# Kernel tuning notes

Measured on AMD Instinct MI355X. Metric: run time of the kernel, lower is better.

The kernel has to match this reference:

```python
import jax, jax.numpy as jnp
import numpy as np

NEG_INF = -9e15
LEAKY_SLOPE = 0.01  # PyTorch F.leaky_relu default


def setup_inputs() -> dict:
    key = jax.random.key(0)
    k1, k2, k3, k4 = jax.random.split(key, 4)
    B, N, Fin, Fout = 4, 4096, 64, 64
    X = jax.random.normal(k1, (B, N, Fin), dtype=jnp.float32)
    A = jax.random.randint(k2, (N, N), 0, 2, dtype=jnp.int32)
    weight = jax.random.normal(k3, (Fin, Fout), dtype=jnp.float32) * 0.15
    a = jax.random.normal(k4, (2 * Fout, 1), dtype=jnp.float32) * 0.15
    return {"X": X, "A": A, "weight": weight, "a": a}


def reference(X, A, weight, a):
    B, N, _ = X.shape
    Fout = weight.shape[1]
    # add self loops: A[i,i] = 1
    mask = (A > 0) | jnp.eye(N, dtype=bool)  # [N, N]
    Xw = jnp.matmul(X, weight)  # [B, N, Fout]
    # additive attention: e_ij = leaky_relu(a_l . x_i + a_r . x_j)
    # equivalent to the repeat/cat/matmul in the original, without O(N^2 F) memory
    a_l = a[:Fout, 0]   # [Fout]
    a_r = a[Fout:, 0]   # [Fout]
    left = jnp.einsum('bnf,f->bn', Xw, a_l)   # [B, N]
    right = jnp.einsum('bnf,f->bn', Xw, a_r)  # [B, N]
    e = left[:, :, None] + right[:, None, :]  # [B, N, N]
    e = jnp.where(e >= 0, e, LEAKY_SLOPE * e)
    att = jnp.where(mask[None, :, :], e, NEG_INF)
    att = jax.nn.softmax(att, axis=-1)  # dropout p=0 -> identity
    out = jnp.matmul(att, Xw)  # [B, N, Fout]
    return out
```

## Files before the change

kernel.cpp:

```cpp
#include <hip/hip_runtime.h>
#include <hip/hip_bf16.h>
#include <math.h>

#define BB 4
#define NN 4096
#define FF 64
#define KS (NN / 32)
#define NKW (KS / 4)
#define C0F 3.35462628e-4f
#define C1F 3.35462628e-6f

typedef _Float16 half8 __attribute__((ext_vector_type(8)));
typedef float f32x4 __attribute__((ext_vector_type(4)));

__global__ void k_pack(const int* __restrict__ A, unsigned int* __restrict__ bitsT) {
    int idx = blockIdx.x * 256 + threadIdx.x;
    int row = idx >> 12;
    int col = idx & (NN - 1);
    bool pred = (A[idx] > 0) || (row == col);
    unsigned long long m = __ballot(pred);
    int lane = threadIdx.x & 63;
    if (lane == 0)  bitsT[(size_t)(col >> 5) * NN + row] = (unsigned int)(m & 0xffffffffULL);
    if (lane == 32) bitsT[(size_t)(col >> 5) * NN + row] = (unsigned int)(m >> 32);
}

__global__ __launch_bounds__(256, 2)
void k_pre(const float* __restrict__ X, const float* __restrict__ W,
           const float* __restrict__ avec, _Float16* __restrict__ XwP,
           float2* __restrict__ LE, float2* __restrict__ RE) {
    __shared__ __align__(16) float Wl[64 * 64];
    __shared__ __align__(16) float Xl[32][64];
    __shared__ __align__(16) float T[32][65];
    __shared__ float al[64];
    __shared__ float ar[64];
    const int t = threadIdx.x;
    const int lane = t & 63;
    const int wv = t >> 6;
    const int r0 = blockIdx.x * 32;

    #pragma unroll
    for (int k = 0; k < 16; ++k) Wl[t + k * 256] = W[t + k * 256];
    if (t < 64) { al[t] = avec[t]; ar[t] = avec[64 + t]; }
    {
        const float4* xs = (const float4*)(X + (size_t)r0 * 64);
        float4* xd = (float4*)&Xl[0][0];
        xd[t] = xs[t];
        xd[t + 256] = xs[t + 256];
    }
    __syncthreads();

    float Wreg[64];
    #pragma unroll
    for (int k = 0; k < 64; ++k) Wreg[k] = Wl[k * 64 + lane];

    #pragma unroll
    for (int rr = 0; rr < 8; ++rr) {
        int lrow = wv * 8 + rr;
        int row  = r0 + lrow;
        float a0 = 0.f, a1 = 0.f, a2 = 0.f, a3 = 0.f;
        #pragma unroll
        for (int k = 0; k < 64; k += 4) {
            float4 x = *(const float4*)&Xl[lrow][k];
            a0 = fmaf(x.x, Wreg[k],     a0);
            a1 = fmaf(x.y, Wreg[k + 1], a1);
            a2 = fmaf(x.z, Wreg[k + 2], a2);
            a3 = fmaf(x.w, Wreg[k + 3], a3);
        }
        float acc = (a0 + a1) + (a2 + a3);
        T[lrow][lane] = acc;

        float lv = acc * al[lane];
        float rv = acc * ar[lane];
        #pragma unroll
        for (int off = 32; off; off >>= 1) {
            lv += __shfl_xor(lv, off, 64);
            rv += __shfl_xor(rv, off, 64);
        }
        if (lane == 0) {
            LE[row] = make_float2(lv, __expf(lv - 8.f));
            RE[row] = make_float2(rv, __expf(rv));
        }
    }
    __syncthreads();

    int b  = r0 >> 12;
    int ks = (r0 & (NN - 1)) >> 5;
    int ct = t >> 6;
    int q  = lane >> 4, n = lane & 15;
    half8 h;
    #pragma unroll
    for (int jj = 0; jj < 8; ++jj)
        h[jj] = (_Float16)T[q * 8 + jj][ct * 16 + n];
    *(half8*)&XwP[((((size_t)b * KS + ks) * 4 + ct) * 64 + lane) * 8] = h;
}

__global__ __launch_bounds__(256, 2)
void k_main(const _Float16* __restrict__ XwP, const float2* __restrict__ LE,
            const float2* __restrict__ RE, const unsigned int* __restrict__ bitsT,
            float* __restrict__ out) {
    __shared__ __align__(16) char smem[32768];
    float2* REs = (float2*)smem;
    float (*Lacc)[32][68] = (float (*)[32][68])smem;
    float* Lsum = (float*)(smem + 17408);

    const int t  = threadIdx.x;
    const int b  = blockIdx.y;
    const int i0 = blockIdx.x * 32;

    const int lane = t & 63;
    const int wv   = t >> 6;
    const int lm   = lane & 15;
    const int q    = lane >> 4;

    const int rowa = i0 + lm;
    const int rowb = i0 + 16 + lm;
    const float2 lea = LE[b * NN + rowa];
    const float2 leb = LE[b * NN + rowb];
    const _Float16* xp = XwP + (size_t)b * KS * 2048 + (size_t)lane * 8;

    {
        const float4* rsrc = (const float4*)(RE + (size_t)b * NN);
        float4* rdst = (float4*)REs;
        #pragma unroll
        for (int k = 0; k < 8; ++k) rdst[t + k * 256] = rsrc[t + k * 256];
    }
    __syncthreads();

    f32x4 acca[4], accb[4];
    f32x4 sacca = (f32x4)0.f, saccb = (f32x4)0.f;
    #pragma unroll
    for (int ct = 0; ct < 4; ++ct) { acca[ct] = (f32x4)0.f; accb[ct] = (f32x4)0.f; }
    half8 vones;
    #pragma unroll
    for (int k = 0; k < 8; ++k) vones[k] = (_Float16)1.0f;

    const int ks0 = wv * NKW;

    const _Float16* base = xp + (size_t)ks0 * 2048;
    half8 nb0 = *(const half8*)(base + 0 * 512);
    half8 nb1 = *(const half8*)(base + 1 * 512);
    half8 nb2 = *(const half8*)(base + 2 * 512);
    half8 nb3 = *(const half8*)(base + 3 * 512);
    unsigned int nwa = bitsT[(size_t)ks0 * NN + rowa];
    unsigned int nwb = bitsT[(size_t)ks0 * NN + rowb];

    #pragma unroll 2
    for (int kk = 0; kk < NKW; ++kk) {
        half8 bf0 = nb0, bf1 = nb1, bf2 = nb2, bf3 = nb3;
        unsigned int wa = nwa >> (q * 8);
        unsigned int wb = nwb >> (q * 8);

        {
            int nk = kk + 1 < NKW ? kk + 1 : kk;
            const _Float16* nbase = xp + (size_t)(ks0 + nk) * 2048;
            nb0 = *(const half8*)(nbase + 0 * 512);
            nb1 = *(const half8*)(nbase + 1 * 512);
            nb2 = *(const half8*)(nbase + 2 * 512);
            nb3 = *(const half8*)(nbase + 3 * 512);
            nwa = bitsT[(size_t)(ks0 + nk) * NN + rowa];
            nwb = bitsT[(size_t)(ks0 + nk) * NN + rowb];
        }

        const float4* rp = (const float4*)(REs + (ks0 + kk) * 32 + q * 8);
        float4 ra = rp[0], rb = rp[1], rc = rp[2], rd = rp[3];
        float r8[8]  = {ra.x, ra.z, rb.x, rb.z, rc.x, rc.z, rd.x, rd.z};
        float er8[8] = {ra.y, ra.w, rb.y, rb.w, rc.y, rc.w, rd.y, rd.w};

        half8 a0a, a0b;
        #pragma unroll
        for (int jj = 0; jj < 8; ++jj) {
            float e0 = lea.x + r8[jj];
            float p0 = fmaxf(lea.y * er8[jj], fmaf(e0, C1F, C0F));
            p0 = ((wa >> jj) & 1u) ? p0 : 0.f;
            a0a[jj] = (_Float16)p0;
        }
        acca[0] = __builtin_amdgcn_mfma_f32_16x16x32_f16(a0a, bf0, acca[0], 0, 0, 0);
        acca[1] = __builtin_amdgcn_mfma_f32_16x16x32_f16(a0a, bf1, acca[1], 0, 0, 0);
        acca[2] = __builtin_amdgcn_mfma_f32_16x16x32_f16(a0a, bf2, acca[2], 0, 0, 0);
        acca[3] = __builtin_amdgcn_mfma_f32_16x16x32_f16(a0a, bf3, acca[3], 0, 0, 0);
        sacca   = __builtin_amdgcn_mfma_f32_16x16x32_f16(a0a, vones, sacca, 0, 0, 0);

        #pragma unroll
        for (int jj = 0; jj < 8; ++jj) {
            float e0 = leb.x + r8[jj];
            float p0 = fmaxf(leb.y * er8[jj], fmaf(e0, C1F, C0F));
            p0 = ((wb >> jj) & 1u) ? p0 : 0.f;
            a0b[jj] = (_Float16)p0;
        }
        accb[0] = __builtin_amdgcn_mfma_f32_16x16x32_f16(a0b, bf0, accb[0], 0, 0, 0);
        accb[1] = __builtin_amdgcn_mfma_f32_16x16x32_f16(a0b, bf1, accb[1], 0, 0, 0);
        accb[2] = __builtin_amdgcn_mfma_f32_16x16x32_f16(a0b, bf2, accb[2], 0, 0, 0);
        accb[3] = __builtin_amdgcn_mfma_f32_16x16x32_f16(a0b, bf3, accb[3], 0, 0, 0);
        saccb   = __builtin_amdgcn_mfma_f32_16x16x32_f16(a0b, vones, saccb, 0, 0, 0);
    }

    __syncthreads();

    if (wv >= 2) {
        #pragma unroll
        for (int r = 0; r < 4; ++r) {
            int lrow = q * 4 + r;
            #pragma unroll
            for (int ct = 0; ct < 4; ++ct) {
                Lacc[wv - 2][lrow][ct * 16 + lm]      = acca[ct][r];
                Lacc[wv - 2][16 + lrow][ct * 16 + lm] = accb[ct][r];
            }
            if (lm == 0) {
                Lsum[(wv - 2) * 32 + lrow]      = sacca[r];
                Lsum[(wv - 2) * 32 + 16 + lrow] = saccb[r];
            }
        }
    }
    __syncthreads();
    if (wv < 2) {
        #pragma unroll
        for (int r = 0; r < 4; ++r) {
            int lrow = q * 4 + r;
            #pragma unroll
            for (int ct = 0; ct < 4; ++ct) {
                Lacc[wv][lrow][ct * 16 + lm]      += acca[ct][r];
                Lacc[wv][16 + lrow][ct * 16 + lm] += accb[ct][r];
            }
            if (lm == 0) {
                Lsum[wv * 32 + lrow]      += sacca[r];
                Lsum[wv * 32 + 16 + lrow] += saccb[r];
            }
        }
    }
    __syncthreads();
    #pragma unroll
    for (int it = 0; it < 2; ++it) {
        int idx  = t + it * 256;
        int lrow = idx >> 4;
        int c0   = (idx & 15) * 4;
        float s = Lsum[lrow] + Lsum[32 + lrow];
        float inv = 1.f / s;
        float4 o;
        o.x = (Lacc[0][lrow][c0 + 0] + Lacc[1][lrow][c0 + 0]) * inv;
        o.y = (Lacc[0][lrow][c0 + 1] + Lacc[1][lrow][c0 + 1]) * inv;
        o.z = (Lacc[0][lrow][c0 + 2] + Lacc[1][lrow][c0 + 2]) * inv;
        o.w = (Lacc[0][lrow][c0 + 3] + Lacc[1][lrow][c0 + 3]) * inv;
        *(float4*)&out[((size_t)(b * NN + i0 + lrow) << 6) + c0] = o;
    }
}

extern "C" void kernel_launch(void* const* d_in, const int* in_sizes, int n_in,
                              void* d_out, int out_size, void* d_ws, size_t ws_size,
                              hipStream_t stream) {
    const float* X    = (const float*)d_in[0];
    const int*   A    = (const int*)d_in[1];
    const float* W    = (const float*)d_in[2];
    const float* avec = (const float*)d_in[3];
    float* out = (float*)d_out;

    char* ws = (char*)d_ws;
    size_t off = 0;
    _Float16* XwP = (_Float16*)(ws + off); off += (size_t)BB * NN * FF * 2;
    float2* LE = (float2*)(ws + off);      off += (size_t)BB * NN * 8;
    float2* RE = (float2*)(ws + off);      off += (size_t)BB * NN * 8;
    unsigned int* bitsT = (unsigned int*)(ws + off);
    off += (size_t)KS * NN * 4;
    (void)off; (void)ws_size;

    k_pack<<<NN * NN / 256, 256, 0, stream>>>(A, bitsT);
    k_pre<<<BB * NN / 32, 256, 0, stream>>>(X, W, avec, XwP, LE, RE);
    k_main<<<dim3(NN / 32, BB), 256, 0, stream>>>(XwP, LE, RE, bitsT, out);
}
```

Baseline: 147.4 us.

## Merge mask packing into preprocessing kernel with vectorized uint4 loads

Folds the adjacency bit-packing kernel into the feature preprocessing kernel as extra blocks, removing one launch. The packing path now loads four ints per thread as uint4 and combines nibbles with a few xor shuffles instead of one ballot per element, so it needs a quarter of the threads. The cost is a heavier combined kernel whose shared-memory footprint also applies to the packing blocks, which may lower their occupancy.

```diff
diff --git a/kernel.cpp b/kernel.cpp
--- a/kernel.cpp
+++ b/kernel.cpp
@@ -9,31 +9,46 @@
 #define NKW (KS / 4)
 #define C0F 3.35462628e-4f
 #define C1F 3.35462628e-6f
+#define PREB 512
 
 typedef _Float16 half8 __attribute__((ext_vector_type(8)));
 typedef float f32x4 __attribute__((ext_vector_type(4)));
 
-__global__ void k_pack(const int* __restrict__ A, unsigned int* __restrict__ bitsT) {
-    int idx = blockIdx.x * 256 + threadIdx.x;
-    int row = idx >> 12;
-    int col = idx & (NN - 1);
-    bool pred = (A[idx] > 0) || (row == col);
-    unsigned long long m = __ballot(pred);
-    int lane = threadIdx.x & 63;
-    if (lane == 0)  bitsT[(size_t)(col >> 5) * NN + row] = (unsigned int)(m & 0xffffffffULL);
-    if (lane == 32) bitsT[(size_t)(col >> 5) * NN + row] = (unsigned int)(m >> 32);
-}
-
 __global__ __launch_bounds__(256, 2)
-void k_pre(const float* __restrict__ X, const float* __restrict__ W,
-           const float* __restrict__ avec, _Float16* __restrict__ XwP,
-           float2* __restrict__ LE, float2* __restrict__ RE) {
+void k_prep(const float* __restrict__ X, const float* __restrict__ W,
+            const float* __restrict__ avec, const int* __restrict__ A,
+            _Float16* __restrict__ XwP, float2* __restrict__ LE,
+            float2* __restrict__ RE, unsigned int* __restrict__ bitsT) {
     __shared__ __align__(16) float Wl[64 * 64];
     __shared__ __align__(16) float Xl[32][64];
     __shared__ __align__(16) float T[32][65];
     __shared__ float al[64];
     __shared__ float ar[64];
+
     const int t = threadIdx.x;
+
+    if (blockIdx.x >= PREB) {
+        int pidx = (blockIdx.x - PREB) * 256 + t;
+        int row  = pidx >> 10;
+        int c4   = pidx & 1023;
+        const uint4* A4 = (const uint4*)A;
+        uint4 av = A4[pidx];
+        unsigned int nib = 0;
+        nib |= ((int)av.x > 0) ? 1u : 0u;
+        nib |= ((int)av.y > 0) ? 2u : 0u;
+        nib |= ((int)av.z > 0) ? 4u : 0u;
+        nib |= ((int)av.w > 0) ? 8u : 0u;
+        if (c4 == (row >> 2)) nib |= 1u << (row & 3);
+        int lane = t & 63;
+        unsigned int v = nib << ((lane & 7) * 4);
+        v |= __shfl_xor(v, 1);
+        v |= __shfl_xor(v, 2);
+        v |= __shfl_xor(v, 4);
+        if ((lane & 7) == 0)
+            bitsT[(size_t)(c4 >> 3) * NN + row] = v;
+        return;
+    }
+
     const int lane = t & 63;
     const int wv = t >> 6;
     const int r0 = blockIdx.x * 32;
@@ -262,7 +277,6 @@
     off += (size_t)KS * NN * 4;
     (void)off; (void)ws_size;
 
-    k_pack<<<NN * NN / 256, 256, 0, stream>>>(A, bitsT);
-    k_pre<<<BB * NN / 32, 256, 0, stream>>>(X, W, avec, XwP, LE, RE);
+    k_prep<<<PREB + NN * NN / 1024, 256, 0, stream>>>(X, W, avec, A, XwP, LE, RE, bitsT);
     k_main<<<dim3(NN / 32, BB), 256, 0, stream>>>(XwP, LE, RE, bitsT, out);
 }
```

Result: faster. 130.5 us (-11.5%).
